# Performance work log

Measured on AMD Instinct MI355X. Metric: run time of the kernel, lower is better.

The kernel has to match this reference:

```python
import jax, jax.numpy as jnp
import numpy as np

WS = 8           # window_size
NH = 8           # num_heads
VD = 384         # values_dim
CD = 128         # coords_dim
ID = 384         # inner_dim = inner_ratio * values_dim
HD = ID // NH    # head_dim = 48


def _rel_bias(pos_emb):
    # static Swin relative-position index table, gathers from pos_emb [2*WS-1, 2*WS-1]
    idx = np.array([[x, y] for x in range(WS) for y in range(WS)])
    rel = idx[None, :, :] - idx[:, None, :] + WS - 1  # [64,64,2]
    return pos_emb[rel[:, :, 0], rel[:, :, 1]]        # [64,64]


def _rmsnorm(x, w, eps=1e-6):
    return x * jax.lax.rsqrt(jnp.mean(x * x, axis=-1, keepdims=True) + eps) * w


def _to_windows(t):
    # t: [b, Hp, Wp, D] with feature layout (e H) -> [b, NH, Wh, Ww, WS*WS, e]
    b, Hp, Wp, D = t.shape
    e = D // NH
    t = t.reshape(b, Hp // WS, WS, Wp // WS, WS, e, NH)
    t = t.transpose(0, 6, 1, 3, 2, 4, 5)
    return t.reshape(b, NH, Hp // WS, Wp // WS, WS * WS, e)


def setup_inputs() -> dict:
    key = jax.random.key(0)
    ks = jax.random.split(key, 8)
    B, H, W = 2, 192, 192
    s = 0.02
    return {
        "values": jax.random.normal(ks[0], (B, H, W, VD), jnp.float32),
        "coords": jax.random.normal(ks[1], (B, H, W, CD), jnp.float32),
        "W_vqk": jax.random.normal(ks[2], (VD, 2 * ID), jnp.float32) * s,
        "b_vqk": jnp.zeros((2 * ID,), jnp.float32),
        "g_vqk": jnp.ones((2 * ID,), jnp.float32),
        "W_vv": jax.random.normal(ks[3], (VD, ID), jnp.float32) * s,
        "b_vv": jnp.zeros((ID,), jnp.float32),
        "W_cqk": jax.random.normal(ks[4], (CD, 2 * ID), jnp.float32) * s,
        "b_cqk": jnp.zeros((2 * ID,), jnp.float32),
        "g_cqk": jnp.ones((2 * ID,), jnp.float32),
        "att_lambda": jax.random.normal(ks[5], (1,), jnp.float32),
        "pos_emb": jax.random.normal(ks[6], (2 * WS - 1, 2 * WS - 1), jnp.float32),
        "W_ov": jax.random.normal(ks[7], (ID, VD), jnp.float32) * s,
        "b_ov": jnp.zeros((VD,), jnp.float32),
    }


def reference(values, coords, W_vqk, b_vqk, g_vqk, W_vv, b_vv,
              W_cqk, b_cqk, g_cqk, att_lambda, pos_emb, W_ov, b_ov):
    b, h, w, _ = values.shape  # h, w divisible by WS -> torch F.pad would add 0
    # values path: cat([RMSNorm(Linear_qk(x)), Linear_v(x)]); '(d k)' with k=3
    # means q/k/v are INTERLEAVED along the feature dim (index d*3+k).
    vqk = _rmsnorm(values @ W_vqk + b_vqk, g_vqk)            # [b,h,w,2*ID]
    vv_ = values @ W_vv + b_vv                               # [b,h,w,ID]
    vcat = jnp.concatenate([vqk, vv_], axis=-1).reshape(b, h, w, ID, 3)
    qv, kv, vv = vcat[..., 0], vcat[..., 1], vcat[..., 2]
    # coords path (update_coords=False): interleaved split k=2
    cqk = _rmsnorm(coords @ W_cqk + b_cqk, g_cqk).reshape(b, h, w, ID, 2)
    qc, kc = cqk[..., 0], cqk[..., 1]
    # shifted=True: roll by -WS//2 (NOTE: original never rolls back)
    shift = -(WS // 2)
    roll = lambda t: jnp.roll(t, (shift, shift), axis=(1, 2))
    qv, kv, vv, qc, kc = (_to_windows(roll(t)) for t in (qv, kv, vv, qc, kc))
    # fused value+coord scores with learned lambda
    dots = (jnp.einsum('bHxyie,bHxyje->bHxyij', qv, kv)
            + att_lambda[0] * jnp.einsum('bHxyie,bHxyje->bHxyij', qc, kc)) / np.sqrt(HD)
    dots = dots + _rel_bias(pos_emb)
    # shifted-window masks on last window row / last window column
    s = WS * (WS // 2)
    n = WS * WS
    row_mask = jnp.zeros((n, n), jnp.float32)
    row_mask = row_mask.at[-s:, :-s].set(-jnp.inf).at[:-s, -s:].set(-jnp.inf)
    col_mask = row_mask.reshape(WS, WS, WS, WS).transpose(1, 0, 3, 2).reshape(n, n)
    dots = dots.at[:, :, -1, :].add(row_mask)
    dots = dots.at[:, :, :, -1].add(col_mask)
    att = jax.nn.softmax(dots, axis=-1)
    yv = jnp.einsum('bHxyij,bHxyje->bHxyie', att, vv)  # [b,NH,Wh,Ww,64,HD]
    Wh, Ww = h // WS, w // WS
    # output layout '(H e)' -> heads slow, e fast
    yv = yv.reshape(b, NH, Wh, Ww, WS, WS, HD).transpose(0, 2, 4, 3, 5, 1, 6)
    yv = yv.reshape(b, Wh * WS, Ww * WS, ID)[:, :h, :w, :]
    return yv @ W_ov + b_ov
```

## Files before the change

### kernel.cpp

```cpp
#include <hip/hip_runtime.h>
#include <hip/hip_bf16.h>

typedef __hip_bfloat16 bf16;
typedef __attribute__((ext_vector_type(8))) short bf16x8;
typedef __attribute__((ext_vector_type(4))) float f32x4;

__device__ __forceinline__ float tof(bf16 x){ return __bfloat162float(x); }
__device__ __forceinline__ bf16  tob(float x){ return __float2bfloat16(x); }
__device__ __forceinline__ float bf2f(short s){ return __uint_as_float(((unsigned)(unsigned short)s) << 16); }

__global__ __launch_bounds__(256) void wprep_k(
    const float* __restrict__ W_vqk, const float* __restrict__ W_vv, const float* __restrict__ W_cqk,
    const float* __restrict__ W_ov,  const float* __restrict__ b_vqk, const float* __restrict__ b_vv,
    const float* __restrict__ b_cqk, const float* __restrict__ g_vqk, const float* __restrict__ g_cqk,
    bf16* __restrict__ W1Tp, bf16* __restrict__ WcTp, bf16* __restrict__ WoT,
    float* __restrict__ bP0, float* __restrict__ bPc, float* __restrict__ gvP, float* __restrict__ gcP,
    float* __restrict__ rs_v, float* __restrict__ rs_c, int npix)
{
  int idx = blockIdx.x*256 + threadIdx.x;
  if (idx < 442368) {
    int n = idx/384, k = idx - n*384;
    int role = n/384, rem = n - role*384, h = rem/48, e = rem - (rem/48)*48;
    int c = 24*e + 3*h + role;
    float v = (e < 32) ? W_vqk[k*768 + c] : W_vv[k*384 + (c - 768)];
    W1Tp[n*384 + k] = tob(v);
  } else if (idx < 540672) {
    int q = idx - 442368;
    int n = q >> 7, k = q & 127;
    int role = n/384, rem = n - role*384, h = rem/48, e = rem - (rem/48)*48;
    WcTp[n*128 + k] = tob(W_cqk[k*768 + 16*e + 2*h + role]);
  } else if (idx < 688128) {
    int q = idx - 540672;
    int n = q/384, k = q - n*384;
    WoT[n*384 + k] = tob(W_ov[k*384 + n]);
  } else if (idx < 689280) {
    int n = idx - 688128;
    int role = n/384, rem = n - role*384, h = rem/48, e = rem - (rem/48)*48;
    int c = 24*e + 3*h + role;
    bP0[n] = (e < 32) ? b_vqk[c] : b_vv[c - 768];
  } else if (idx < 690048) {
    int n = idx - 689280;
    int role = n/384, rem = n - role*384, h = rem/48, e = rem - (rem/48)*48;
    bPc[n] = b_cqk[16*e + 2*h + role];
  } else if (idx < 691200) {
    int n = idx - 690048;
    int role = n/384, rem = n - role*384, h = rem/48, e = rem - (rem/48)*48;
    gvP[n] = (e < 32) ? g_vqk[24*e + 3*h + role] : 1.0f;
  } else if (idx < 691968) {
    int n = idx - 691200;
    int role = n/384, rem = n - role*384, h = rem/48, e = rem - (rem/48)*48;
    gcP[n] = g_cqk[16*e + 2*h + role];
  } else if (idx < 691968 + 2*npix) {
    int q = idx - 691968;
    if (q < npix) rs_v[q] = 0.f; else rs_c[q - npix] = 0.f;
  }
}

template<int MODE>
__global__ __launch_bounds__(256,4) void gemm_k(const float* __restrict__ Af, const bf16* __restrict__ Ab,
    const bf16* __restrict__ WT, const float* __restrict__ biasP,
    bf16* __restrict__ outb, float* __restrict__ outf, float* __restrict__ rsum,
    float* __restrict__ z0, float* __restrict__ z1, int bb, int row0, int pix0)
{
  constexpr int KTOT = (MODE==1) ? 128 : 384;
  constexpr int NT   = (MODE==0) ? 1152 : (MODE==1) ? 768 : 384;
  constexpr int BM   = (MODE==2) ? 64 : 128;
  constexpr int MT4  = BM/32;
  constexpr int ACH  = BM*8;
  __shared__ bf16 As[128][72];
  __shared__ bf16 Bs[128][72];
  const int tid = threadIdx.x, lane = tid & 63, wid = tid >> 6;
  const int wr = (wid >> 1)*(BM/2), wc = (wid & 1)*64;
  const int rowbase = blockIdx.x*BM;
  const int nbase   = blockIdx.y*128;

  if constexpr (MODE == 2) {
    if (blockIdx.y == 0) {
      if (tid < 64) z0[rowbase + tid] = 0.f;
      else if (tid < 128) z1[rowbase + tid - 64] = 0.f;
    }
  }

  f32x4 acc[MT4][4] = {};
  for (int ks = 0; ks < KTOT; ks += 64) {
    __syncthreads();
    #pragma unroll
    for (int it = 0; it < (ACH + 1024)/256; it++) {
      int idx = it*256 + tid;
      if (idx < ACH) {
        int r = idx >> 3, c = idx & 7;
        if constexpr (MODE == 2) {
          *(uint4*)&As[r][c*8] = *(const uint4*)(Ab + (size_t)(rowbase + r)*KTOT + ks + c*8);
        } else {
          int pix = rowbase + r;
          int lr = pix/192, lc = pix - (pix/192)*192;
          int srow = (row0 + lr + 4) % 192;
          int scol = (lc + 4) % 192;
          const float* src = Af + (((size_t)bb*192 + srow)*192 + scol)*KTOT + ks + c*8;
          float4 f0 = *(const float4*)src;
          float4 f1 = *(const float4*)(src + 4);
          union { bf16 h[8]; uint4 u4; } t;
          t.h[0]=tob(f0.x); t.h[1]=tob(f0.y); t.h[2]=tob(f0.z); t.h[3]=tob(f0.w);
          t.h[4]=tob(f1.x); t.h[5]=tob(f1.y); t.h[6]=tob(f1.z); t.h[7]=tob(f1.w);
          *(uint4*)&As[r][c*8] = t.u4;
        }
      } else {
        int q = idx - ACH; int r = q >> 3, c = q & 7;
        *(uint4*)&Bs[r][c*8] = *(const uint4*)(WT + (size_t)(nbase + r)*KTOT + ks + c*8);
      }
    }
    __syncthreads();
    #pragma unroll
    for (int k2 = 0; k2 < 64; k2 += 32) {
      const int kb = k2 + (lane >> 4)*8, ml = lane & 15;
      bf16x8 a[MT4], b[4];
      #pragma unroll
      for (int t = 0; t < MT4; t++) a[t] = *(const bf16x8*)&As[wr + t*16 + ml][kb];
      #pragma unroll
      for (int t = 0; t < 4; t++)  b[t] = *(const bf16x8*)&Bs[wc + t*16 + ml][kb];
      #pragma unroll
      for (int mt = 0; mt < MT4; mt++)
      #pragma unroll
      for (int nt = 0; nt < 4; nt++)
        acc[mt][nt] = __builtin_amdgcn_mfma_f32_16x16x32_bf16(a[mt], b[nt], acc[mt][nt], 0, 0, 0);
    }
  }
  const int lr4 = (lane >> 4)*4, lcol = lane & 15;
  if constexpr (MODE == 2) {
    #pragma unroll
    for (int mt = 0; mt < MT4; mt++)
    #pragma unroll
    for (int nt = 0; nt < 4; nt++) {
      f32x4 av = acc[mt][nt];
      int n = nbase + wc + nt*16 + lcol;
      float bv = biasP[n];
      #pragma unroll
      for (int i = 0; i < 4; i++) {
        int pix = rowbase + wr + mt*16 + lr4 + i;
        outf[(size_t)(pix0 + pix)*384 + n] = av[i] + bv;
      }
    }
  } else {
    __syncthreads();
    bf16* Crow = (wc == 0) ? &As[0][0] : &Bs[0][0];
    #pragma unroll
    for (int mt = 0; mt < MT4; mt++) {
      #pragma unroll
      for (int i = 0; i < 4; i++) {
        int row = wr + mt*16 + lr4 + i;
        int pix = rowbase + row;
        float sq_ = 0.f;
        #pragma unroll
        for (int nt = 0; nt < 4; nt++) {
          int n = nbase + wc + nt*16 + lcol;
          float v = acc[mt][nt][i] + biasP[n];
          Crow[row*72 + nt*16 + lcol] = tob(v);
          if (MODE == 1 || (n % 48) < 32) sq_ += v*v;
        }
        sq_ += __shfl_xor(sq_, 1); sq_ += __shfl_xor(sq_, 2);
        sq_ += __shfl_xor(sq_, 4); sq_ += __shfl_xor(sq_, 8);
        if (lcol == 0) atomicAdd(&rsum[pix], sq_);
      }
    }
    __syncthreads();
    #pragma unroll
    for (int u = 0; u < 8; u++) {
      int q = u*256 + tid;
      int half = q >> 10, idx = q & 1023, r = idx >> 3, s = idx & 7;
      const bf16* srcp = half ? &Bs[r][s*8] : &As[r][s*8];
      *(uint4*)(outb + (size_t)(rowbase + r)*NT + nbase + half*64 + s*8) = *(const uint4*)srcp;
    }
  }
}

__device__ __forceinline__ bf16x8 pack8g(uint4 raw, float r, float4 ga, float4 gb)
{
  union { uint4 u4; unsigned short us[8]; } rw; rw.u4 = raw;
  union { bf16x8 v; bf16 h[8]; } o;
  o.h[0] = tob(bf2f((short)rw.us[0]) * (r * ga.x));
  o.h[1] = tob(bf2f((short)rw.us[1]) * (r * ga.y));
  o.h[2] = tob(bf2f((short)rw.us[2]) * (r * ga.z));
  o.h[3] = tob(bf2f((short)rw.us[3]) * (r * ga.w));
  o.h[4] = tob(bf2f((short)rw.us[4]) * (r * gb.x));
  o.h[5] = tob(bf2f((short)rw.us[5]) * (r * gb.y));
  o.h[6] = tob(bf2f((short)rw.us[6]) * (r * gb.z));
  o.h[7] = tob(bf2f((short)rw.us[7]) * (r * gb.w));
  return o.v;
}

__device__ __forceinline__ float rmsf(float s){ return rsqrtf(s*(1.f/768.f) + 1e-6f); }

__global__ __launch_bounds__(256,4) void attn_k(const bf16* __restrict__ Y0, const bf16* __restrict__ Yc,
    const float* __restrict__ rs_v, const float* __restrict__ rs_c,
    const float* __restrict__ gvP, const float* __restrict__ gcP,
    const float* __restrict__ lam_p, const float* __restrict__ pos,
    bf16* __restrict__ y_att, int row0)
{
  __shared__ bf16 Ks[64][104];
  __shared__ bf16 Vt[48][72];
  __shared__ bf16 Pb[64][72];
  __shared__ float sq[96];
  __shared__ float poss[225];
  const int tid = threadIdx.x, lane = tid & 63, w = tid >> 6;
  const int win = blockIdx.x, h = blockIdx.y;
  const int wx = win/24, wy = win - (win/24)*24;
  const float lam = lam_p[0];
  const float SCL = 0.14433756729740643f;

  if (tid < 96) sq[tid] = (tid < 48 ? gvP[h*48 + tid] : gcP[h*48 + tid - 48]*lam) * SCL;
  if (tid < 225) poss[tid] = pos[tid];

  {
    const int j = lane;
    const int p = (wx*8 + (j>>3))*192 + wy*8 + (j&7);
    const float rvj = rmsf(rs_v[p]), rcj = rmsf(rs_c[p]);
    for (int grp = w; grp < 18; grp += 4) {
      if (grp < 6) {
        int c = grp;
        uint4 raw = *(const uint4*)(Y0 + (size_t)p*1152 + 384 + h*48 + c*8);
        const float* gp = gvP + 384 + h*48 + c*8;
        float4 ga = *(const float4*)gp, gb = *(const float4*)(gp+4);
        float r = (c < 4) ? rvj : 1.0f;
        union { bf16x8 v; uint4 u4; } o; o.v = pack8g(raw, r, ga, gb);
        *(uint4*)&Ks[j][c*8] = o.u4;
      } else if (grp < 12) {
        int c = grp - 6;
        uint4 raw = *(const uint4*)(Yc + (size_t)p*768 + 384 + h*48 + c*8);
        const float* gp = gcP + 384 + h*48 + c*8;
        float4 ga = *(const float4*)gp, gb = *(const float4*)(gp+4);
        union { bf16x8 v; uint4 u4; } o; o.v = pack8g(raw, rcj, ga, gb);
        *(uint4*)&Ks[j][48 + c*8] = o.u4;
      } else {
        int c = grp - 12;
        uint4 raw = *(const uint4*)(Y0 + (size_t)p*1152 + 768 + h*48 + c*8);
        const float* gp = gvP + 768 + h*48 + c*8;
        float4 ga = *(const float4*)gp, gb = *(const float4*)(gp+4);
        float r = (c < 4) ? rvj : 1.0f;
        union { uint4 u4; unsigned short us[8]; } rw; rw.u4 = raw;
        Vt[c*8+0][j] = tob(bf2f((short)rw.us[0]) * (r * ga.x));
        Vt[c*8+1][j] = tob(bf2f((short)rw.us[1]) * (r * ga.y));
        Vt[c*8+2][j] = tob(bf2f((short)rw.us[2]) * (r * ga.z));
        Vt[c*8+3][j] = tob(bf2f((short)rw.us[3]) * (r * ga.w));
        Vt[c*8+4][j] = tob(bf2f((short)rw.us[4]) * (r * gb.x));
        Vt[c*8+5][j] = tob(bf2f((short)rw.us[5]) * (r * gb.y));
        Vt[c*8+6][j] = tob(bf2f((short)rw.us[6]) * (r * gb.z));
        Vt[c*8+7][j] = tob(bf2f((short)rw.us[7]) * (r * gb.w));
      }
    }
  }
  __syncthreads();

  const int ml = lane & 15, k0 = (lane >> 4)*8;
  const int mrow = w*16 + ml;
  const int pA = (wx*8 + (mrow>>3))*192 + wy*8 + (mrow&7);
  const float rvA = rmsf(rs_v[pA]), rcA = rmsf(rs_c[pA]);
  bf16x8 qf0, qf1, qf2;
  {
    uint4 r0 = *(const uint4*)(Y0 + (size_t)pA*1152 + h*48 + k0);
    float4 ga = *(const float4*)&sq[k0],      gb = *(const float4*)&sq[k0+4];
    qf0 = pack8g(r0, rvA, ga, gb);
    const bf16* s1 = (k0 < 16) ? (Y0 + (size_t)pA*1152 + h*48 + 32 + k0)
                               : (Yc + (size_t)pA*768  + h*48 + (k0 - 16));
    float r1 = (k0 < 16) ? 1.0f : rcA;
    uint4 raw1 = *(const uint4*)s1;
    ga = *(const float4*)&sq[32+k0]; gb = *(const float4*)&sq[36+k0];
    qf1 = pack8g(raw1, r1, ga, gb);
    uint4 r2 = *(const uint4*)(Yc + (size_t)pA*768 + h*48 + 16 + k0);
    ga = *(const float4*)&sq[64+k0]; gb = *(const float4*)&sq[68+k0];
    qf2 = pack8g(r2, rcA, ga, gb);
  }

  f32x4 acc[4] = {};
  #pragma unroll
  for (int nt = 0; nt < 4; nt++) {
    bf16x8 b0 = *(const bf16x8*)&Ks[nt*16 + ml][k0];
    bf16x8 b1 = *(const bf16x8*)&Ks[nt*16 + ml][32 + k0];
    bf16x8 b2 = *(const bf16x8*)&Ks[nt*16 + ml][64 + k0];
    acc[nt] = __builtin_amdgcn_mfma_f32_16x16x32_bf16(qf0, b0, acc[nt], 0, 0, 0);
    acc[nt] = __builtin_amdgcn_mfma_f32_16x16x32_bf16(qf1, b1, acc[nt], 0, 0, 0);
    acc[nt] = __builtin_amdgcn_mfma_f32_16x16x32_bf16(qf2, b2, acc[nt], 0, 0, 0);
  }

  const bool rowm = ((row0 >> 3) + wx) == 23;
  const bool colm = (wy == 23);
  const int g4 = (lane >> 4)*4;
  float pv[4][4];
  float inv_[4];
  #pragma unroll
  for (int i = 0; i < 4; i++) {
    int r = w*16 + g4 + i;
    int txi = r >> 3, tyi = r & 7;
    #pragma unroll
    for (int nt = 0; nt < 4; nt++) {
      int j = nt*16 + ml;
      int txj = j >> 3, tyj = j & 7;
      float v = acc[nt][i] + poss[(txj - txi + 7)*15 + (tyj - tyi + 7)];
      if ((rowm && ((txi >= 4) != (txj >= 4))) || (colm && ((tyi >= 4) != (tyj >= 4)))) v = -1e30f;
      pv[i][nt] = v;
    }
    float mx = fmaxf(fmaxf(pv[i][0], pv[i][1]), fmaxf(pv[i][2], pv[i][3]));
    #pragma unroll
    for (int m = 1; m < 16; m <<= 1) mx = fmaxf(mx, __shfl_xor(mx, m));
    float s0 = 0.f;
    #pragma unroll
    for (int nt = 0; nt < 4; nt++) { pv[i][nt] = __expf(pv[i][nt] - mx); s0 += pv[i][nt]; }
    #pragma unroll
    for (int m = 1; m < 16; m <<= 1) s0 += __shfl_xor(s0, m);
    inv_[i] = 1.f / s0;
  }
  #pragma unroll
  for (int i = 0; i < 4; i++)
  #pragma unroll
  for (int nt = 0; nt < 4; nt++)
    Pb[w*16 + g4 + i][nt*16 + ml] = tob(pv[i][nt]);

  f32x4 o0 = {}, o1 = {}, o2 = {};
  {
    bf16x8 a0 = *(const bf16x8*)&Pb[w*16 + ml][k0];
    bf16x8 b;
    b = *(const bf16x8*)&Vt[ 0 + ml][k0];      o0 = __builtin_amdgcn_mfma_f32_16x16x32_bf16(a0, b, o0, 0, 0, 0);
    b = *(const bf16x8*)&Vt[16 + ml][k0];      o1 = __builtin_amdgcn_mfma_f32_16x16x32_bf16(a0, b, o1, 0, 0, 0);
    b = *(const bf16x8*)&Vt[32 + ml][k0];      o2 = __builtin_amdgcn_mfma_f32_16x16x32_bf16(a0, b, o2, 0, 0, 0);
    bf16x8 a1 = *(const bf16x8*)&Pb[w*16 + ml][32 + k0];
    b = *(const bf16x8*)&Vt[ 0 + ml][32 + k0]; o0 = __builtin_amdgcn_mfma_f32_16x16x32_bf16(a1, b, o0, 0, 0, 0);
    b = *(const bf16x8*)&Vt[16 + ml][32 + k0]; o1 = __builtin_amdgcn_mfma_f32_16x16x32_bf16(a1, b, o1, 0, 0, 0);
    b = *(const bf16x8*)&Vt[32 + ml][32 + k0]; o2 = __builtin_amdgcn_mfma_f32_16x16x32_bf16(a1, b, o2, 0, 0, 0);
  }

  #pragma unroll
  for (int i = 0; i < 4; i++) {
    Pb[w*16 + g4 + i][     ml] = tob(o0[i] * inv_[i]);
    Pb[w*16 + g4 + i][16 + ml] = tob(o1[i] * inv_[i]);
    Pb[w*16 + g4 + i][32 + ml] = tob(o2[i] * inv_[i]);
  }
  #pragma unroll
  for (int s2 = 0; s2 < 3; s2++) {
    int u = s2*64 + lane;
    int row = u / 12, seg = u - row*12;
    int rr = w*16 + row;
    int pC = (wx*8 + (rr>>3))*192 + wy*8 + (rr&7);
    uint2 d = *(const uint2*)&Pb[rr][seg*4];
    *(uint2*)(y_att + (size_t)pC*384 + h*48 + seg*4) = d;
  }
}

extern "C" void kernel_launch(void* const* d_in, const int* in_sizes, int n_in,
                              void* d_out, int out_size, void* d_ws, size_t ws_size,
                              hipStream_t stream)
{
  const float* values = (const float*)d_in[0];
  const float* coords = (const float*)d_in[1];
  const float* W_vqk  = (const float*)d_in[2];
  const float* b_vqk  = (const float*)d_in[3];
  const float* g_vqk  = (const float*)d_in[4];
  const float* W_vv   = (const float*)d_in[5];
  const float* b_vv   = (const float*)d_in[6];
  const float* W_cqk  = (const float*)d_in[7];
  const float* b_cqk  = (const float*)d_in[8];
  const float* g_cqk  = (const float*)d_in[9];
  const float* lam    = (const float*)d_in[10];
  const float* pos    = (const float*)d_in[11];
  const float* W_ov   = (const float*)d_in[12];
  const float* b_ov   = (const float*)d_in[13];
  float* out = (float*)d_out;
  (void)in_sizes; (void)n_in; (void)out_size;

  const size_t FIX = 1391616;
  size_t need_full = FIX + (size_t)36864*1152*2 + (size_t)36864*768*2 + 2*(size_t)36864*4 + (size_t)36864*384*2;
  const bool full = (ws_size >= need_full);
  const int nrows = full ? 192 : 64;
  const int npix  = nrows*192;

  char* ws = (char*)d_ws;
  bf16*  W1Tp  = (bf16*)(ws + 0);
  bf16*  WcTp  = (bf16*)(ws + 884736);
  bf16*  WoT   = (bf16*)(ws + 1081344);
  float* bP0   = (float*)(ws + 1376256);
  float* bPc   = (float*)(ws + 1380864);
  float* gvP   = (float*)(ws + 1383936);
  float* gcP   = (float*)(ws + 1388544);
  size_t off = FIX;
  bf16*  Y0    = (bf16*)(ws + off);  off += (size_t)npix*1152*2;
  bf16*  Yc    = (bf16*)(ws + off);  off += (size_t)npix*768*2;
  float* rs_v  = (float*)(ws + off); off += (size_t)npix*4;
  float* rs_c  = (float*)(ws + off); off += (size_t)npix*4;
  bf16*  y_att = (bf16*)(ws + off);

  int wgrid = (691968 + 2*npix + 255)/256;
  wprep_k<<<wgrid, 256, 0, stream>>>(W_vqk, W_vv, W_cqk, W_ov, b_vqk, b_vv, b_cqk, g_vqk, g_cqk,
                                     W1Tp, WcTp, WoT, bP0, bPc, gvP, gcP, rs_v, rs_c, npix);

  const int nreg = full ? 2 : 6;
  for (int rg = 0; rg < nreg; rg++) {
    int bb   = full ? rg : rg/3;
    int row0 = full ? 0  : (rg - bb*3)*64;
    int pix0 = bb*36864 + row0*192;
    dim3 gq(npix/128, 9), gc(npix/128, 6), ga((nrows/8)*24, 8), go(npix/64, 3);
    gemm_k<0><<<gq, 256, 0, stream>>>(values, nullptr, W1Tp, bP0, Y0, nullptr, rs_v,
                                      nullptr, nullptr, bb, row0, 0);
    gemm_k<1><<<gc, 256, 0, stream>>>(coords, nullptr, WcTp, bPc, Yc, nullptr, rs_c,
                                      nullptr, nullptr, bb, row0, 0);
    attn_k<<<ga, 256, 0, stream>>>(Y0, Yc, rs_v, rs_c, gvP, gcP, lam, pos, y_att, row0);
    gemm_k<2><<<go, 256, 0, stream>>>(nullptr, y_att, WoT, b_ov, nullptr, out, nullptr,
                                      rs_v, rs_c, 0, 0, pix0);
  }
}
```

Before: 608.5 us.

## Prefetch next K-slice of GEMM operands into registers during MFMA compute

After: 839.3 us. +37.9%, slower.

```diff
diff --git a/kernel.cpp b/kernel.cpp
--- a/kernel.cpp
+++ b/kernel.cpp
@@ -57,7 +57,8 @@
 }
 
 template<int MODE>
-__global__ __launch_bounds__(256,4) void gemm_k(const float* __restrict__ Af, const bf16* __restrict__ Ab,
+__global__ __launch_bounds__(256, (MODE==2) ? 4 : 3) void gemm_k(
+    const float* __restrict__ Af, const bf16* __restrict__ Ab,
     const bf16* __restrict__ WT, const float* __restrict__ biasP,
     bf16* __restrict__ outb, float* __restrict__ outf, float* __restrict__ rsum,
     float* __restrict__ z0, float* __restrict__ z1, int bb, int row0, int pix0)
@@ -66,7 +67,7 @@
   constexpr int NT   = (MODE==0) ? 1152 : (MODE==1) ? 768 : 384;
   constexpr int BM   = (MODE==2) ? 64 : 128;
   constexpr int MT4  = BM/32;
-  constexpr int ACH  = BM*8;
+  constexpr int AIT  = BM*8/256;
   __shared__ bf16 As[128][72];
   __shared__ bf16 Bs[128][72];
   const int tid = threadIdx.x, lane = tid & 63, wid = tid >> 6;
@@ -81,35 +82,68 @@
     }
   }
 
+  unsigned abase[AIT], bbase[4];
+  #pragma unroll
+  for (int it = 0; it < AIT; it++) {
+    int idx = it*256 + tid, r = idx >> 3, c = idx & 7;
+    if constexpr (MODE == 2) {
+      abase[it] = (unsigned)((rowbase + r)*KTOT + c*8);
+    } else {
+      int pix = rowbase + r;
+      int lr = pix/192, lc = pix - (pix/192)*192;
+      int srow = (row0 + lr + 4) % 192;
+      int scol = (lc + 4) % 192;
+      abase[it] = (unsigned)(((bb*192 + srow)*192 + scol)*KTOT + c*8);
+    }
+  }
+  #pragma unroll
+  for (int it = 0; it < 4; it++) {
+    int idx = it*256 + tid, r = idx >> 3, c = idx & 7;
+    bbase[it] = (unsigned)((nbase + r)*KTOT + c*8);
+  }
+
+  float4 paf[(MODE==2)?1:AIT][2];
+  uint4  pab[(MODE==2)?AIT:1];
+  uint4  pb[4];
+
+  #pragma unroll
+  for (int it = 0; it < AIT; it++) {
+    if constexpr (MODE == 2) pab[it] = *(const uint4*)(Ab + abase[it]);
+    else { const float* s = Af + abase[it]; paf[it][0] = *(const float4*)s; paf[it][1] = *(const float4*)(s+4); }
+  }
+  #pragma unroll
+  for (int it = 0; it < 4; it++) pb[it] = *(const uint4*)(WT + bbase[it]);
+
   f32x4 acc[MT4][4] = {};
   for (int ks = 0; ks < KTOT; ks += 64) {
+    #pragma unroll
+    for (int it = 0; it < AIT; it++) {
+      int idx = it*256 + tid, r = idx >> 3, c = idx & 7;
+      if constexpr (MODE == 2) {
+        *(uint4*)&As[r][c*8] = pab[it];
+      } else {
+        union { bf16 h[8]; uint4 u4; } t;
+        t.h[0]=tob(paf[it][0].x); t.h[1]=tob(paf[it][0].y); t.h[2]=tob(paf[it][0].z); t.h[3]=tob(paf[it][0].w);
+        t.h[4]=tob(paf[it][1].x); t.h[5]=tob(paf[it][1].y); t.h[6]=tob(paf[it][1].z); t.h[7]=tob(paf[it][1].w);
+        *(uint4*)&As[r][c*8] = t.u4;
+      }
+    }
+    #pragma unroll
+    for (int it = 0; it < 4; it++) {
+      int idx = it*256 + tid, r = idx >> 3, c = idx & 7;
+      *(uint4*)&Bs[r][c*8] = pb[it];
+    }
     __syncthreads();
-    #pragma unroll
-    for (int it = 0; it < (ACH + 1024)/256; it++) {
-      int idx = it*256 + tid;
-      if (idx < ACH) {
-        int r = idx >> 3, c = idx & 7;
-        if constexpr (MODE == 2) {
-          *(uint4*)&As[r][c*8] = *(const uint4*)(Ab + (size_t)(rowbase + r)*KTOT + ks + c*8);
-        } else {
-          int pix = rowbase + r;
-          int lr = pix/192, lc = pix - (pix/192)*192;
-          int srow = (row0 + lr + 4) % 192;
-          int scol = (lc + 4) % 192;
-          const float* src = Af + (((size_t)bb*192 + srow)*192 + scol)*KTOT + ks + c*8;
-          float4 f0 = *(const float4*)src;
-          float4 f1 = *(const float4*)(src + 4);
-          union { bf16 h[8]; uint4 u4; } t;
-          t.h[0]=tob(f0.x); t.h[1]=tob(f0.y); t.h[2]=tob(f0.z); t.h[3]=tob(f0.w);
-          t.h[4]=tob(f1.x); t.h[5]=tob(f1.y); t.h[6]=tob(f1.z); t.h[7]=tob(f1.w);
-          *(uint4*)&As[r][c*8] = t.u4;
-        }
-      } else {
-        int q = idx - ACH; int r = q >> 3, c = q & 7;
-        *(uint4*)&Bs[r][c*8] = *(const uint4*)(WT + (size_t)(nbase + r)*KTOT + ks + c*8);
+    if (ks + 64 < KTOT) {
+      #pragma unroll
+      for (int it = 0; it < AIT; it++) {
+        if constexpr (MODE == 2) pab[it] = *(const uint4*)(Ab + abase[it] + ks + 64);
+        else { const float* s = Af + abase[it] + ks + 64;
+               paf[it][0] = *(const float4*)s; paf[it][1] = *(const float4*)(s+4); }
       }
-    }
-    __syncthreads();
+      #pragma unroll
+      for (int it = 0; it < 4; it++) pb[it] = *(const uint4*)(WT + bbase[it] + ks + 64);
+    }
     #pragma unroll
     for (int k2 = 0; k2 < 64; k2 += 32) {
       const int kb = k2 + (lane >> 4)*8, ml = lane & 15;
@@ -124,6 +158,7 @@
       for (int nt = 0; nt < 4; nt++)
         acc[mt][nt] = __builtin_amdgcn_mfma_f32_16x16x32_bf16(a[mt], b[nt], acc[mt][nt], 0, 0, 0);
     }
+    __syncthreads();
   }
   const int lr4 = (lane >> 4)*4, lcol = lane & 15;
   if constexpr (MODE == 2) {
@@ -141,7 +176,6 @@
       }
     }
   } else {
-    __syncthreads();
     bf16* Crow = (wc == 0) ? &As[0][0] : &Bs[0][0];
     #pragma unroll
     for (int mt = 0; mt < MT4; mt++) {
```
